# Kernel tuning notes

Measured on AMD Instinct MI355X. Metric: run time of the kernel, lower is better.

Reference implementation:

```python
import jax, jax.numpy as jnp
import numpy as np

L, B, N, C, H = 8, 8, 512, 1024, 16
D = C // H
TP = (2.0 * D) ** 0.5  # temperature_coeff * head_dim, sqrt


def _ln(x):
    # LayerNorm(eps=1e-6, no affine)
    m = jnp.mean(x, axis=-1, keepdims=True)
    v = jnp.var(x, axis=-1, keepdims=True)
    return (x - m) * jax.lax.rsqrt(v + 1e-6)


def _modulate(x, shift, scale):
    return x * (1 + scale) + shift


def setup_inputs() -> dict:
    key = jax.random.key(0)
    ks = jax.random.split(key, 18)
    s = 0.02
    return {
        "x": jax.random.normal(ks[0], (B, N, C), dtype=jnp.float32),
        "time": jax.random.uniform(ks[1], (B, 1), dtype=jnp.float32) * 100.0,
        "label": jax.random.normal(ks[2], (B, 2), dtype=jnp.float32),
        "x_mask": jax.random.randint(ks[3], (B, N, 1), 0, 2).astype(jnp.float32),
        # ValueLabelEmbed: Linear(2 -> C)
        "Wl": jax.random.normal(ks[4], (C, 2), dtype=jnp.float32) * s,
        "bl": jnp.zeros((C,), dtype=jnp.float32),
        # per-layer stacked weights (leading dim L)
        "Wq": jax.random.normal(ks[5], (L, C, C), dtype=jnp.float32) * s,
        "Wk": jax.random.normal(ks[6], (L, C, C), dtype=jnp.float32) * s,
        "Wv": jax.random.normal(ks[7], (L, C, C), dtype=jnp.float32) * s,
        "W1": jax.random.normal(ks[8], (L, 4 * C, C), dtype=jnp.float32) * s,
        "b1": jnp.zeros((L, 4 * C), dtype=jnp.float32),
        "W2": jax.random.normal(ks[9], (L, C, 4 * C), dtype=jnp.float32) * s,
        "b2": jnp.zeros((L, C), dtype=jnp.float32),
        "Wm": jax.random.normal(ks[10], (L, 6 * C, C), dtype=jnp.float32) * s,
        "bm": jnp.zeros((L, 6 * C), dtype=jnp.float32),
        # FinalLayer
        "Wf": jax.random.normal(ks[11], (C, C), dtype=jnp.float32) * s,
        "bf": jnp.zeros((C,), dtype=jnp.float32),
        "Wmf": jax.random.normal(ks[12], (2 * C, C), dtype=jnp.float32) * s,
        "bmf": jnp.zeros((2 * C,), dtype=jnp.float32),
    }


def reference(x, time, label, x_mask, Wl, bl, Wq, Wk, Wv, W1, b1, W2, b2, Wm, bm, Wf, bf, Wmf, bmf):
    # ValueLabelEmbed: (B,2) -> (B,1,C)
    lemb = (label @ Wl.T + bl)[:, None, :]
    # TimeEmbedding: interleaved sin/cos of time / 10000^(2i/d)
    base = jnp.power(10000.0, 2.0 * jnp.arange(C, dtype=jnp.float32) / C)
    te = time / base  # (B, C)
    even = (jnp.arange(C) % 2) == 0
    te = jnp.where(even, jnp.sin(te), jnp.cos(te))
    c = lemb + te[:, None, :]  # (B,1,C)

    # self-attention mask: True where exactly one of the pair is valid
    xm = x_mask[:, :, 0]  # (B,N)
    mask = ((xm[:, :, None] + xm[:, None, :]) == 1.0)[:, None, :, :]  # (B,1,N,N)

    def block(xc, p):
        wq, wk, wv, w1, bb1, w2, bb2, wm, bbm = p
        m6 = jax.nn.selu(c) @ wm.T + bbm  # (B,1,6C)
        sm, sc, gm, sf, cf, gf = jnp.split(m6, 6, axis=-1)
        h = _modulate(_ln(xc), sm, sc) * x_mask
        q = (h @ wq.T).reshape(B, N, H, D)
        k = (h @ wk.T).reshape(B, N, H, D)
        v = (h @ wv.T).reshape(B, N, H, D)
        scores = jnp.einsum('bqhd,bkhd->bhqk', q, k) / TP
        scores = jnp.where(mask, -jnp.inf, scores)
        alpha = jax.nn.softmax(scores, axis=-1)
        att = jnp.einsum('bhqk,bkhd->bqhd', alpha, v).reshape(B, N, C)
        xc = xc + gm * att
        h2 = _modulate(_ln(xc), sf, cf)
        ffn = jax.nn.selu(h2 @ w1.T + bb1) @ w2.T + bb2
        xc = (xc + gf * ffn) * x_mask
        return xc, None

    x, _ = jax.lax.scan(block, x, (Wq, Wk, Wv, W1, b1, W2, b2, Wm, bm))

    # FinalLayer
    m2 = jax.nn.selu(c) @ Wmf.T + bmf
    shift, scale = jnp.split(m2, 2, axis=-1)
    out = (_modulate(_ln(x), shift, scale) @ Wf.T + bf) * x_mask
    return out
```

## Files before the change

### kernel.cpp

```cpp
#include <hip/hip_runtime.h>
#include <hip/hip_bf16.h>
#include <cstddef>

#define DEVI __device__ __forceinline__

typedef __attribute__((ext_vector_type(4))) float f4v;
typedef __attribute__((ext_vector_type(16))) float f16v;
typedef __attribute__((ext_vector_type(8))) short s8v;
typedef __attribute__((ext_vector_type(4))) short s4v;

using bf16 = __hip_bfloat16;

constexpr float SELU_A = 1.6732632423543772f;
constexpr float SELU_S = 1.0507009873554805f;
constexpr float TPINV  = 0.08838834764831845f;

DEVI float bfbits(short s) { return __uint_as_float(((unsigned)(unsigned short)s) << 16); }
DEVI unsigned short f2bu(float f) {
  bf16 h = __float2bfloat16(f);
  return __builtin_bit_cast(unsigned short, h);
}
DEVI float seluf(float x) { return x > 0.f ? SELU_S * x : SELU_S * SELU_A * (__expf(x) - 1.f); }

DEVI void gl16(const void* g, void* l) {
  __builtin_amdgcn_global_load_lds((__attribute__((address_space(1))) void*)g,
                                   (__attribute__((address_space(3))) void*)l, 16, 0, 0);
}

DEVI void conv8(const float* __restrict__ src, bf16* __restrict__ dst) {
  f4v a = *(const f4v*)src;
  f4v b = *(const f4v*)(src + 4);
  s8v o;
  #pragma unroll
  for (int j = 0; j < 4; j++) { o[j] = (short)f2bu(a[j]); o[4 + j] = (short)f2bu(b[j]); }
  *(s8v*)dst = o;
}

__global__ void k_compact(const float* __restrict__ xm, int* __restrict__ idx,
                          int* __restrict__ pos, int* __restrict__ cnt,
                          int* __restrict__ start, int* __restrict__ t2b)
{
  int t = threadIdx.x;
  int b = t >> 6, lane = t & 63;
  __shared__ int scnt[8];
  int base = b * 512 + lane * 8;
  int mb[8]; int lc = 0;
  #pragma unroll
  for (int i = 0; i < 8; i++) { mb[i] = (xm[base + i] != 0.f) ? 1 : 0; lc += mb[i]; }
  int s = lc;
  #pragma unroll
  for (int o = 1; o < 64; o <<= 1) { int tt = __shfl_up(s, o); if (lane >= o) s += tt; }
  int run = s - lc;
  #pragma unroll
  for (int i = 0; i < 8; i++) {
    int n = lane * 8 + i;
    if (mb[i]) { idx[b * 512 + run] = n; pos[b * 512 + n] = run; run++; }
    else pos[b * 512 + n] = -1;
  }
  if (lane == 63) scnt[b] = s;
  __syncthreads();
  if (t == 0) {
    int st = 0, tile = 0;
    for (int bb = 0; bb < 8; bb++) {
      cnt[bb] = scnt[bb];
      start[bb] = st;
      int nt = (scnt[bb] + 127) >> 7;
      for (int k = 0; k < nt * 2; k++) t2b[tile++] = bb;
      st += nt * 128;
    }
    start[8] = st;
    for (; tile < 64; tile++) t2b[tile] = 0;
  }
}

__global__ __launch_bounds__(256) void k_prolog(
    const float* __restrict__ xin, const int* __restrict__ idx, const int* __restrict__ cnt,
    const int* __restrict__ start, const int* __restrict__ t2b, float* __restrict__ xc,
    const float* __restrict__ wq, const float* __restrict__ wk, const float* __restrict__ wv,
    const float* __restrict__ w1, const float* __restrict__ w2,
    bf16* __restrict__ wqkvb, bf16* __restrict__ w1b, bf16* __restrict__ w2b,
    const float* __restrict__ cs, const float* __restrict__ Wm, const float* __restrict__ bm,
    float* __restrict__ mAll, const float* __restrict__ Wmf, const float* __restrict__ bmf,
    float* __restrict__ m2v)
{
  int bid = blockIdx.x, t = threadIdx.x;
  __shared__ float cls[8192];
  if (bid < 4096) {
    int row = bid;
    if (row >= start[8]) return;
    int tb = t2b[row >> 6], slot = row - start[tb];
    f4v v = {0.f, 0.f, 0.f, 0.f};
    if (slot < cnt[tb])
      v = *(const f4v*)&xin[((size_t)tb * 512 + idx[tb * 512 + slot]) * 1024 + t * 4];
    *(f4v*)&xc[(size_t)row * 1024 + t * 4] = v;
  } else if (bid < 9728) {
    int i = (bid - 4096) * 256 + t;
    if (i < 393216) {
      int o = i * 8;
      int row = o >> 10, col = o & 1023;
      int sel = row >> 10, sr = row & 1023;
      conv8((sel == 0 ? wq : sel == 1 ? wk : wv) + (size_t)sr * 1024 + col, wqkvb + o);
    } else if (i < 917504) {
      size_t o = (size_t)(i - 393216) * 8;
      conv8(w1 + o, w1b + o);
    } else {
      size_t o = (size_t)(i - 917504) * 8;
      conv8(w2 + o, w2b + o);
    }
  } else {
    int mode = (bid < 22016) ? 0 : 1;
    const float* W = mode ? Wmf : Wm;
    const float* bias = mode ? bmf : bm;
    float* out = mode ? m2v : mAll;
    int O = mode ? 2048 : 49152;
    int ob = mode ? (bid - 22016) : (bid - 9728);
    #pragma unroll
    for (int i = 0; i < 8; i++)
      *(f4v*)&cls[i * 1024 + t * 4] = *(const f4v*)&cs[i * 1024 + t * 4];
    __syncthreads();
    int w = t >> 6, l = t & 63;
    int o = ob * 4 + w;
    if (o >= O) return;
    const float* Wr = W + (size_t)o * 1024;
    f4v wv[4];
    #pragma unroll
    for (int i = 0; i < 4; i++) wv[i] = *(const f4v*)&Wr[i * 256 + l * 4];
    float acc[8] = {0.f, 0.f, 0.f, 0.f, 0.f, 0.f, 0.f, 0.f};
    #pragma unroll
    for (int i = 0; i < 4; i++) {
      #pragma unroll
      for (int b = 0; b < 8; b++) {
        f4v cv = *(const f4v*)&cls[b * 1024 + i * 256 + l * 4];
        acc[b] += wv[i][0] * cv[0] + wv[i][1] * cv[1] + wv[i][2] * cv[2] + wv[i][3] * cv[3];
      }
    }
    #pragma unroll
    for (int b = 0; b < 8; b++) {
      #pragma unroll
      for (int off = 32; off; off >>= 1) acc[b] += __shfl_xor(acc[b], off);
    }
    float bv = bias[o];
    #pragma unroll
    for (int b = 0; b < 8; b++) {
      if (l == b) {
        float val = acc[b] + bv;
        size_t dst;
        if (mode == 0) { int ll = o / 6144, ft = o - ll * 6144; dst = ((size_t)ll * 8 + b) * 6144 + ft; }
        else dst = (size_t)b * 2048 + o;
        out[dst] = val;
      }
    }
  }
}

__global__ __launch_bounds__(256) void k_scatter(const float* __restrict__ ffin,
    const int* __restrict__ pos, const int* __restrict__ start, float* __restrict__ out)
{
  int row = blockIdx.x, t = threadIdx.x, b = row >> 9;
  int p = pos[row];
  f4v v = {0.f, 0.f, 0.f, 0.f};
  if (p >= 0) v = *(const f4v*)&ffin[(size_t)(start[b] + p) * 1024 + t * 4];
  *(f4v*)&out[(size_t)row * 1024 + t * 4] = v;
}

__global__ void k_cond(const float* __restrict__ tim, const float* __restrict__ lab,
                       const float* __restrict__ Wl, const float* __restrict__ bl,
                       float* __restrict__ cs)
{
  int b = blockIdx.x, t = threadIdx.x;
  float l0 = lab[b * 2 + 0], l1 = lab[b * 2 + 1], tv = tim[b];
  #pragma unroll
  for (int i = 0; i < 4; i++) {
    int j = t + 256 * i;
    float e = powf(10000.f, (2.f * (float)j) * (1.f / 1024.f));
    float arg = tv / e;
    float te = ((j & 1) == 0) ? sinf(arg) : cosf(arg);
    float c = l0 * Wl[j * 2 + 0] + l1 * Wl[j * 2 + 1] + bl[j] + te;
    cs[b * 1024 + j] = seluf(c);
  }
}

__global__ __launch_bounds__(256) void k_lnmod(
    const float* __restrict__ x, const float* __restrict__ shiftB, const float* __restrict__ scaleB,
    int bstride, const int* __restrict__ cnt, const int* __restrict__ start,
    const int* __restrict__ t2b, bf16* __restrict__ out)
{
  int row = blockIdx.x, t = threadIdx.x;
  if (row >= start[8]) return;
  int tb = t2b[row >> 6], slot = row - start[tb];
  if (slot >= cnt[tb]) {
    s4v z = {0, 0, 0, 0};
    *(s4v*)&out[(size_t)row * 1024 + t * 4] = z;
    return;
  }
  const float* xr = x + (size_t)row * 1024;
  f4v v = *(const f4v*)&xr[t * 4];
  float s = v[0] + v[1] + v[2] + v[3];
  float ss = v[0]*v[0] + v[1]*v[1] + v[2]*v[2] + v[3]*v[3];
  #pragma unroll
  for (int off = 32; off; off >>= 1) { s += __shfl_xor(s, off); ss += __shfl_xor(ss, off); }
  __shared__ float rs[4], rss[4];
  int w = t >> 6;
  if ((t & 63) == 0) { rs[w] = s; rss[w] = ss; }
  __syncthreads();
  s = rs[0] + rs[1] + rs[2] + rs[3];
  ss = rss[0] + rss[1] + rss[2] + rss[3];
  float mean = s * (1.f / 1024.f);
  float var = ss * (1.f / 1024.f) - mean * mean;
  float rstd = rsqrtf(var + 1e-6f);
  f4v sh = *(const f4v*)&shiftB[(size_t)tb * bstride + t * 4];
  f4v sc = *(const f4v*)&scaleB[(size_t)tb * bstride + t * 4];
  s4v o;
  #pragma unroll
  for (int i = 0; i < 4; i++)
    o[i] = (short)f2bu((v[i] - mean) * rstd * (1.f + sc[i]) + sh[i]);
  *(s4v*)&out[(size_t)row * 1024 + t * 4] = o;
}

__global__ __launch_bounds__(256) void k_resid(
    float* __restrict__ x, const bf16* __restrict__ att, const float* __restrict__ m6b,
    const int* __restrict__ cnt, const int* __restrict__ start,
    const int* __restrict__ t2b, bf16* __restrict__ h2)
{
  int row = blockIdx.x, t = threadIdx.x;
  if (row >= start[8]) return;
  int tb = t2b[row >> 6], slot = row - start[tb];
  if (slot >= cnt[tb]) {
    s4v z = {0, 0, 0, 0};
    *(s4v*)&h2[(size_t)row * 1024 + t * 4] = z;
    return;
  }
  float* xr = x + (size_t)row * 1024;
  const float* gm = m6b + (size_t)tb * 6144 + 2048;
  const float* sf = m6b + (size_t)tb * 6144 + 3072;
  const float* cf = m6b + (size_t)tb * 6144 + 4096;
  f4v xv = *(const f4v*)&xr[t * 4];
  s4v av = *(const s4v*)&att[((size_t)tb * 512 + slot) * 1024 + t * 4];
  f4v gv = *(const f4v*)&gm[t * 4];
  f4v vv;
  #pragma unroll
  for (int i = 0; i < 4; i++) vv[i] = xv[i] + gv[i] * bfbits(av[i]);
  *(f4v*)&xr[t * 4] = vv;
  float s = vv[0] + vv[1] + vv[2] + vv[3];
  float ss = vv[0]*vv[0] + vv[1]*vv[1] + vv[2]*vv[2] + vv[3]*vv[3];
  #pragma unroll
  for (int off = 32; off; off >>= 1) { s += __shfl_xor(s, off); ss += __shfl_xor(ss, off); }
  __shared__ float rs[4], rss[4];
  int w = t >> 6;
  if ((t & 63) == 0) { rs[w] = s; rss[w] = ss; }
  __syncthreads();
  s = rs[0] + rs[1] + rs[2] + rs[3];
  ss = rss[0] + rss[1] + rss[2] + rss[3];
  float mean = s * (1.f / 1024.f);
  float var = ss * (1.f / 1024.f) - mean * mean;
  float rstd = rsqrtf(var + 1e-6f);
  f4v sfv = *(const f4v*)&sf[t * 4];
  f4v cfv = *(const f4v*)&cf[t * 4];
  s4v o;
  #pragma unroll
  for (int i = 0; i < 4; i++)
    o[i] = (short)f2bu((vv[i] - mean) * rstd * (1.f + cfv[i]) + sfv[i]);
  *(s4v*)&h2[(size_t)row * 1024 + t * 4] = o;
}

__global__ __launch_bounds__(256) void k_attn(
    const bf16* __restrict__ q, const bf16* __restrict__ k, const bf16* __restrict__ vt,
    const int* __restrict__ cnt, bf16* __restrict__ att,
    const float* __restrict__ nwq, const float* __restrict__ nwk, const float* __restrict__ nwv,
    const float* __restrict__ nw1, const float* __restrict__ nw2,
    bf16* __restrict__ dqkv, bf16* __restrict__ dw1, bf16* __restrict__ dw2, int mode)
{
  if (blockIdx.x >= 4) {
    int cid = (blockIdx.x - 4) * 128 + blockIdx.y;
    int i0 = cid * 256 + threadIdx.x;
    #pragma unroll
    for (int half = 0; half < 2; half++) {
      int j = i0 * 2 + half;
      if (mode == 1) {
        if (j < 131072) conv8(nwq + (size_t)j * 8, dqkv + (size_t)j * 8);
      } else {
        if (j < 393216) {
          int o = j * 8;
          int row = o >> 10, col = o & 1023;
          int sel = row >> 10, sr = row & 1023;
          conv8((sel == 0 ? nwq : sel == 1 ? nwk : nwv) + (size_t)sr * 1024 + col, dqkv + o);
        } else if (j < 917504) {
          size_t o = (size_t)(j - 393216) * 8;
          conv8(nw1 + o, dw1 + o);
        } else {
          size_t o = (size_t)(j - 917504) * 8;
          conv8(nw2 + o, dw2 + o);
        }
      }
    }
    return;
  }

  int bh = blockIdx.y, b = bh >> 4, hh = bh & 15;
  int cntb = cnt[b];
  if ((int)blockIdx.x * 128 >= cntb) return;
  int t = threadIdx.x, w = t >> 6, lane = t & 63;
  int fr = lane & 15, g = lane >> 4;
  int qw = blockIdx.x * 128 + w * 32;
  const size_t ho = (size_t)bh * (512 * 64);

  __shared__ bf16 Pb[4][32][72];

  s8v qf[2][2];
  #pragma unroll
  for (int mf = 0; mf < 2; mf++)
    #pragma unroll
    for (int kk = 0; kk < 2; kk++)
      qf[mf][kk] = *(const s8v*)(q + ho + (size_t)(qw + mf * 16 + fr) * 64 + kk * 32 + g * 8);

  float mrow[2][4], lsum[2][4];
  f4v oacc[2][4];
  const f4v vzero = {0.f, 0.f, 0.f, 0.f};
  #pragma unroll
  for (int mf = 0; mf < 2; mf++)
    #pragma unroll
    for (int r = 0; r < 4; r++) { mrow[mf][r] = -3.0e38f; lsum[mf][r] = 0.f; }
  #pragma unroll
  for (int mf = 0; mf < 2; mf++)
    #pragma unroll
    for (int nd = 0; nd < 4; nd++) oacc[mf][nd] = vzero;

  int nkt = (cntb + 63) >> 6;
  for (int kt = 0; kt < nkt; kt++) {
    int kb0 = kt * 64;
    f4v sacc[2][4];
    #pragma unroll
    for (int mf = 0; mf < 2; mf++)
      #pragma unroll
      for (int nf = 0; nf < 4; nf++) sacc[mf][nf] = vzero;
    #pragma unroll
    for (int kk = 0; kk < 2; kk++) {
      s8v kf[4];
      #pragma unroll
      for (int nf = 0; nf < 4; nf++)
        kf[nf] = *(const s8v*)(k + ho + (size_t)(kb0 + nf * 16 + fr) * 64 + kk * 32 + g * 8);
      #pragma unroll
      for (int mf = 0; mf < 2; mf++)
        #pragma unroll
        for (int nf = 0; nf < 4; nf++)
          sacc[mf][nf] = __builtin_amdgcn_mfma_f32_16x16x32_bf16(qf[mf][kk], kf[nf], sacc[mf][nf], 0, 0, 0);
    }
    #pragma unroll
    for (int mf = 0; mf < 2; mf++) {
      #pragma unroll
      for (int r = 0; r < 4; r++) {
        float mx = -3.0e38f;
        #pragma unroll
        for (int nf = 0; nf < 4; nf++) {
          float s = sacc[mf][nf][r] * TPINV;
          if (kb0 + nf * 16 + fr >= cntb) s = -1.0e30f;
          sacc[mf][nf][r] = s;
          mx = fmaxf(mx, s);
        }
        mx = fmaxf(mx, __shfl_xor(mx, 1));
        mx = fmaxf(mx, __shfl_xor(mx, 2));
        mx = fmaxf(mx, __shfl_xor(mx, 4));
        mx = fmaxf(mx, __shfl_xor(mx, 8));
        float mnew = fmaxf(mrow[mf][r], mx);
        float corr = __expf(mrow[mf][r] - mnew);
        mrow[mf][r] = mnew;
        float ps = 0.f;
        #pragma unroll
        for (int nf = 0; nf < 4; nf++) {
          float p = __expf(sacc[mf][nf][r] - mnew);
          ps += p;
          Pb[w][mf * 16 + g * 4 + r][nf * 16 + fr] = __float2bfloat16(p);
        }
        lsum[mf][r] = lsum[mf][r] * corr + ps;
        #pragma unroll
        for (int nd = 0; nd < 4; nd++) oacc[mf][nd][r] *= corr;
      }
    }
    #pragma unroll
    for (int kk = 0; kk < 2; kk++) {
      s8v pf[2], vf[4];
      #pragma unroll
      for (int mf = 0; mf < 2; mf++)
        pf[mf] = *(const s8v*)&Pb[w][mf * 16 + fr][kk * 32 + g * 8];
      #pragma unroll
      for (int nd = 0; nd < 4; nd++)
        vf[nd] = *(const s8v*)(vt + ho + (size_t)(nd * 16 + fr) * 512 + kb0 + kk * 32 + g * 8);
      #pragma unroll
      for (int mf = 0; mf < 2; mf++)
        #pragma unroll
        for (int nd = 0; nd < 4; nd++)
          oacc[mf][nd] = __builtin_amdgcn_mfma_f32_16x16x32_bf16(pf[mf], vf[nd], oacc[mf][nd], 0, 0, 0);
    }
  }
  float inv[2][4];
  #pragma unroll
  for (int mf = 0; mf < 2; mf++)
    #pragma unroll
    for (int r = 0; r < 4; r++) {
      float ls = lsum[mf][r];
      ls += __shfl_xor(ls, 1);
      ls += __shfl_xor(ls, 2);
      ls += __shfl_xor(ls, 4);
      ls += __shfl_xor(ls, 8);
      inv[mf][r] = 1.f / ls;
    }
  #pragma unroll
  for (int mf = 0; mf < 2; mf++)
    #pragma unroll
    for (int nd = 0; nd < 4; nd++)
      #pragma unroll
      for (int r = 0; r < 4; r++) {
        int row = qw + mf * 16 + g * 4 + r;
        att[(size_t)(b * 512 + row) * 1024 + hh * 64 + nd * 16 + fr] =
            __float2bfloat16(oacc[mf][nd][r] * inv[mf][r]);
      }
}

template <int EPI, int BM, int BN>
__global__ __launch_bounds__(256) void k_gemm(
    const bf16* __restrict__ A, const bf16* __restrict__ W,
    const float* __restrict__ bias, int Kst, int kLen, int Ncols,
    const int* __restrict__ cnt, const int* __restrict__ start, const int* __restrict__ t2b,
    bf16* __restrict__ outb, float* __restrict__ outf)
{
  constexpr int MFR = BM / 64;
  constexpr int NFR = BN / 64;
  constexpr int NA  = BM / 32;
  constexpr int NW  = BN / 32;
  __shared__ bf16 As[BM][64];
  __shared__ bf16 Ws[BN][64];
  int t = threadIdx.x, lane = t & 63, w = t >> 6;
  int wr = w >> 1, wc = w & 1;
  int m0 = blockIdx.y * BM, n0 = blockIdx.x * BN;
  if (m0 >= start[8]) return;
  int kOff = blockIdx.z * kLen;
  int r32 = lane & 31, hi = lane >> 5;

  const bf16* Abase = A + (size_t)m0 * Kst + kOff;
  const bf16* Wbase = W + (size_t)n0 * Kst + kOff;

  f16v acc[MFR][NFR];
  #pragma unroll
  for (int i = 0; i < MFR; i++)
    #pragma unroll
    for (int j = 0; j < NFR; j++)
      #pragma unroll
      for (int e = 0; e < 16; e++) acc[i][j][e] = 0.f;

  int nkt = kLen >> 6;
  for (int kt = 0; kt < nkt; kt++) {
    int k0 = kt << 6;
    __syncthreads();
    #pragma unroll
    for (int i = 0; i < NA; i++) {
      int Z = w * (NA * 1024) + i * 1024 + lane * 16;
      int row = Z >> 7, slot = (Z >> 4) & 7;
      int ss = slot ^ (row & 7);
      gl16(Abase + (size_t)row * Kst + k0 + ss * 8, (char*)As + Z);
    }
    #pragma unroll
    for (int i = 0; i < NW; i++) {
      int Z = w * (NW * 1024) + i * 1024 + lane * 16;
      int row = Z >> 7, slot = (Z >> 4) & 7;
      int ss = slot ^ (row & 7);
      gl16(Wbase + (size_t)row * Kst + k0 + ss * 8, (char*)Ws + Z);
    }
    __syncthreads();
    #pragma unroll
    for (int kk = 0; kk < 4; kk++) {
      s8v af[MFR], bfr[NFR];
      #pragma unroll
      for (int mf = 0; mf < MFR; mf++) {
        int row = wr * (BM / 2) + mf * 32 + r32;
        int sl = (kk * 2 + hi) ^ (row & 7);
        af[mf] = *(const s8v*)((const char*)As + row * 128 + sl * 16);
      }
      #pragma unroll
      for (int nf = 0; nf < NFR; nf++) {
        int row = wc * (BN / 2) + nf * 32 + r32;
        int sl = (kk * 2 + hi) ^ (row & 7);
        bfr[nf] = *(const s8v*)((const char*)Ws + row * 128 + sl * 16);
      }
      #pragma unroll
      for (int mf = 0; mf < MFR; mf++)
        #pragma unroll
        for (int nf = 0; nf < NFR; nf++)
          acc[mf][nf] = __builtin_amdgcn_mfma_f32_32x32x16_bf16(af[mf], bfr[nf], acc[mf][nf], 0, 0, 0);
    }
  }

  int tb = t2b[m0 >> 6];
  int sb = start[tb];
  #pragma unroll
  for (int mf = 0; mf < MFR; mf++) {
    #pragma unroll
    for (int nf = 0; nf < NFR; nf++) {
      int col = n0 + wc * (BN / 2) + nf * 32 + r32;
      #pragma unroll
      for (int qd = 0; qd < 4; qd++) {
        int row0 = m0 + wr * (BM / 2) + mf * 32 + qd * 8 + hi * 4;
        if (EPI == 0) {
          int sel = col >> 10, cl = col & 1023;
          int nn = row0 - sb;
          int h2 = cl >> 6, dd = cl & 63;
          if (sel == 2) {
            s4v o4;
            #pragma unroll
            for (int r = 0; r < 4; r++) o4[r] = (short)f2bu(acc[mf][nf][qd * 4 + r]);
            *(s4v*)&outb[(size_t)2 * 4194304 + (((size_t)tb * 16 + h2) * 64 + dd) * 512 + nn] = o4;
          } else {
            #pragma unroll
            for (int r = 0; r < 4; r++)
              outb[(size_t)sel * 4194304 + (((size_t)tb * 16 + h2) * 512 + (nn + r)) * 64 + dd] =
                  __float2bfloat16(acc[mf][nf][qd * 4 + r]);
          }
        } else {
          #pragma unroll
          for (int r = 0; r < 4; r++) {
            int row = row0 + r;
            float val = acc[mf][nf][qd * 4 + r];
            if (EPI == 1) {
              outb[(size_t)row * Ncols + col] = __float2bfloat16(seluf(val + bias[col]));
            } else if (EPI == 3) {
              outf[(size_t)row * 1024 + col] = val + bias[col];
            } else {
              outb[(size_t)blockIdx.z * 4194304 + (size_t)row * 1024 + col] = __float2bfloat16(val);
            }
          }
        }
      }
    }
  }
}

__global__ __launch_bounds__(256) void k_comb(
    const bf16* __restrict__ part, const float* __restrict__ bias,
    const float* __restrict__ gfb, const float* __restrict__ shiftN,
    const float* __restrict__ scaleN, int strideN,
    float* __restrict__ x, const int* __restrict__ cnt, const int* __restrict__ start,
    const int* __restrict__ t2b, bf16* __restrict__ h)
{
  int row = blockIdx.x, t = threadIdx.x;
  if (row >= start[8]) return;
  int tb = t2b[row >> 6], slot = row - start[tb];
  if (slot >= cnt[tb]) return;
  size_t o = (size_t)row * 1024 + t * 4;
  f4v sum = {0.f, 0.f, 0.f, 0.f};
  #pragma unroll
  for (int p = 0; p < 8; p++) {
    s4v pv = *(const s4v*)&part[o + (size_t)p * 4194304];
    #pragma unroll
    for (int i = 0; i < 4; i++) sum[i] += bfbits(pv[i]);
  }
  f4v bv = *(const f4v*)&bias[t * 4];
  f4v gf = *(const f4v*)&gfb[(size_t)tb * 6144 + t * 4];
  f4v xv = *(const f4v*)&x[o];
  f4v vv;
  #pragma unroll
  for (int i = 0; i < 4; i++)
    vv[i] = xv[i] + gf[i] * (sum[i] + bv[i]);
  *(f4v*)&x[o] = vv;
  float s = vv[0] + vv[1] + vv[2] + vv[3];
  float ss = vv[0]*vv[0] + vv[1]*vv[1] + vv[2]*vv[2] + vv[3]*vv[3];
  #pragma unroll
  for (int off = 32; off; off >>= 1) { s += __shfl_xor(s, off); ss += __shfl_xor(ss, off); }
  __shared__ float rs[4], rss[4];
  int w = t >> 6;
  if ((t & 63) == 0) { rs[w] = s; rss[w] = ss; }
  __syncthreads();
  s = rs[0] + rs[1] + rs[2] + rs[3];
  ss = rss[0] + rss[1] + rss[2] + rss[3];
  float mean = s * (1.f / 1024.f);
  float var = ss * (1.f / 1024.f) - mean * mean;
  float rstd = rsqrtf(var + 1e-6f);
  f4v sh = *(const f4v*)&shiftN[(size_t)tb * strideN + t * 4];
  f4v sc = *(const f4v*)&scaleN[(size_t)tb * strideN + t * 4];
  s4v ho;
  #pragma unroll
  for (int i = 0; i < 4; i++)
    ho[i] = (short)f2bu((vv[i] - mean) * rstd * (1.f + sc[i]) + sh[i]);
  *(s4v*)&h[(size_t)row * 1024 + t * 4] = ho;
}

extern "C" void kernel_launch(void* const* d_in, const int* in_sizes, int n_in,
                              void* d_out, int out_size, void* d_ws, size_t ws_size,
                              hipStream_t stream)
{
  const float* x_in  = (const float*)d_in[0];
  const float* tim   = (const float*)d_in[1];
  const float* lab   = (const float*)d_in[2];
  const float* xmask = (const float*)d_in[3];
  const float* Wl  = (const float*)d_in[4];
  const float* bl  = (const float*)d_in[5];
  const float* Wq  = (const float*)d_in[6];
  const float* Wk  = (const float*)d_in[7];
  const float* Wv  = (const float*)d_in[8];
  const float* W1  = (const float*)d_in[9];
  const float* b1  = (const float*)d_in[10];
  const float* W2  = (const float*)d_in[11];
  const float* b2  = (const float*)d_in[12];
  const float* Wm  = (const float*)d_in[13];
  const float* bm  = (const float*)d_in[14];
  const float* Wf  = (const float*)d_in[15];
  const float* bfp = (const float*)d_in[16];
  const float* Wmf = (const float*)d_in[17];
  const float* bmf = (const float*)d_in[18];

  char* ws = (char*)d_ws;
  float* x     = (float*)(ws + 0);
  float* cs    = (float*)(ws + 16777216);
  float* mAll  = (float*)(ws + 16809984);
  float* m2v   = (float*)(ws + 18382848);
  bf16*  h     = (bf16*)(ws + 18448384);
  bf16*  qb    = (bf16*)(ws + 26836992);
  bf16*  kb    = (bf16*)(ws + 35225600);
  bf16*  vb    = (bf16*)(ws + 43614208);
  bf16*  att   = (bf16*)(ws + 52002816);
  bf16*  f1    = (bf16*)(ws + 60391424);
  bf16*  wqkv0 = (bf16*)(ws + 93945856);
  bf16*  w1b0  = (bf16*)(ws + 100237312);
  bf16*  w2b0  = (bf16*)(ws + 108625920);
  bf16*  wfb   = (bf16*)(ws + 117014528);
  float* ffin  = (float*)(ws + 119111680);
  int*   idxb  = (int*)(ws + 135888896);
  int*   posb  = (int*)(ws + 135905280);
  int*   cntb  = (int*)(ws + 135921664);
  int*   strtb = (int*)(ws + 135921728);
  int*   t2bb  = (int*)(ws + 135921792);
  bf16*  wqkv1 = (bf16*)(ws + 135925760);
  bf16*  w1b1  = (bf16*)(ws + 142217216);
  bf16*  w2b1  = (bf16*)(ws + 150605824);
  bf16*  part  = (bf16*)(ws + 158994432);

  bf16* wqkvS[2] = { wqkv0, wqkv1 };
  bf16* w1S[2]   = { w1b0, w1b1 };
  bf16* w2S[2]   = { w2b0, w2b1 };

  k_compact<<<1, 512, 0, stream>>>(xmask, idxb, posb, cntb, strtb, t2bb);
  k_cond<<<8, 256, 0, stream>>>(tim, lab, Wl, bl, cs);
  k_prolog<<<22528, 256, 0, stream>>>(x_in, idxb, cntb, strtb, t2bb, x,
                                      Wq, Wk, Wv, W1, W2, wqkv0, w1b0, w2b0,
                                      cs, Wm, bm, mAll, Wmf, bmf, m2v);
  k_lnmod<<<4096, 256, 0, stream>>>(x, mAll + 0, mAll + 1024, 6144, cntb, strtb, t2bb, h);

  for (int l = 0; l < 8; l++) {
    const float* m6b = mAll + (size_t)l * 49152;
    int sel = l & 1, nsel = sel ^ 1;
    int last = (l == 7);

    k_gemm<0, 128, 64><<<dim3(48, 32), 256, 0, stream>>>(h, wqkvS[sel], nullptr, 1024, 1024, 3072,
                                                         cntb, strtb, t2bb, qb, nullptr);
    if (!last) {
      k_attn<<<dim3(26, 128), 256, 0, stream>>>(qb, kb, vb, cntb, att,
          Wq + (size_t)(l + 1) * 1048576, Wk + (size_t)(l + 1) * 1048576,
          Wv + (size_t)(l + 1) * 1048576, W1 + (size_t)(l + 1) * 4194304,
          W2 + (size_t)(l + 1) * 4194304,
          wqkvS[nsel], w1S[nsel], w2S[nsel], 0);
    } else {
      k_attn<<<dim3(26, 128), 256, 0, stream>>>(qb, kb, vb, cntb, att,
          Wf, Wf, Wf, Wf, Wf, wfb, wfb, wfb, 1);
    }
    k_resid<<<4096, 256, 0, stream>>>(x, att, m6b, cntb, strtb, t2bb, h);
    k_gemm<1, 128, 64><<<dim3(64, 32), 256, 0, stream>>>(h, w1S[sel], b1 + l * 4096, 1024, 1024, 4096,
                                                         cntb, strtb, t2bb, f1, nullptr);
    k_gemm<4, 128, 128><<<dim3(8, 32, 8), 256, 0, stream>>>(f1, w2S[sel], nullptr, 4096, 512, 1024,
                                                            cntb, strtb, t2bb, part, nullptr);
    const float* nShift = last ? m2v : (mAll + (size_t)(l + 1) * 49152);
    const float* nScale = last ? (m2v + 1024) : (mAll + (size_t)(l + 1) * 49152 + 1024);
    int nStride = last ? 2048 : 6144;
    k_comb<<<4096, 256, 0, stream>>>(part, b2 + l * 1024, m6b + 5120,
                                     nShift, nScale, nStride,
                                     x, cntb, strtb, t2bb, h);
  }

  k_gemm<3, 128, 64><<<dim3(16, 32), 256, 0, stream>>>(h, wfb, bfp, 1024, 1024, 1024,
                                                       cntb, strtb, t2bb, nullptr, ffin);
  k_scatter<<<4096, 256, 0, stream>>>(ffin, posb, strtb, (float*)d_out);
}
```

Measured before the change: 1.357 ms.

## Defer per-layer modulation matvecs into attention kernel and batch rows per wave

The prologue no longer computes all eight layers' modulation vectors (Wm @ selu(c)). It now computes only layer 0 and the final-layer vector. Each later layer's modulation matvec is computed by extra blocks appended to the previous layer's attention launch, alongside the bf16 weight conversions already placed there. The matvec helper also processes four output rows per wave instead of one, which cuts the number of blocks and how often the conditioning vector is staged into LDS. The shared-memory buffer is unified so the attention scratch and the conditioning vector share one allocation. The cost is more register pressure in the matvec and slightly larger attention grids.

```diff
diff --git a/kernel.cpp b/kernel.cpp
--- a/kernel.cpp
+++ b/kernel.cpp
@@ -34,6 +34,42 @@
   #pragma unroll
   for (int j = 0; j < 4; j++) { o[j] = (short)f2bu(a[j]); o[4 + j] = (short)f2bu(b[j]); }
   *(s8v*)dst = o;
+}
+
+DEVI void matvec16(const float* __restrict__ W, const float* __restrict__ bias,
+                   float* __restrict__ out, const float* cls, int base, int O, int stride)
+{
+  int t = threadIdx.x, w = t >> 6, l = t & 63;
+  int o0 = base + w * 4;
+  if (o0 >= O) return;
+  f4v wv[4][4];
+  #pragma unroll
+  for (int r = 0; r < 4; r++)
+    #pragma unroll
+    for (int i = 0; i < 4; i++)
+      wv[r][i] = *(const f4v*)&W[(size_t)(o0 + r) * 1024 + i * 256 + l * 4];
+  #pragma unroll
+  for (int r = 0; r < 4; r++) {
+    float acc[8] = {0.f, 0.f, 0.f, 0.f, 0.f, 0.f, 0.f, 0.f};
+    #pragma unroll
+    for (int i = 0; i < 4; i++) {
+      #pragma unroll
+      for (int b = 0; b < 8; b++) {
+        f4v cv = *(const f4v*)&cls[b * 1024 + i * 256 + l * 4];
+        acc[b] += wv[r][i][0] * cv[0] + wv[r][i][1] * cv[1] +
+                  wv[r][i][2] * cv[2] + wv[r][i][3] * cv[3];
+      }
+    }
+    #pragma unroll
+    for (int b = 0; b < 8; b++) {
+      #pragma unroll
+      for (int off = 32; off; off >>= 1) acc[b] += __shfl_xor(acc[b], off);
+    }
+    float bv = bias[o0 + r];
+    #pragma unroll
+    for (int b = 0; b < 8; b++)
+      if (l == b) out[(size_t)b * stride + o0 + r] = acc[b] + bv;
+  }
 }
 
 __global__ void k_compact(const float* __restrict__ xm, int* __restrict__ idx,
@@ -108,48 +144,14 @@
       conv8(w2 + o, w2b + o);
     }
   } else {
-    int mode = (bid < 22016) ? 0 : 1;
-    const float* W = mode ? Wmf : Wm;
-    const float* bias = mode ? bmf : bm;
-    float* out = mode ? m2v : mAll;
-    int O = mode ? 2048 : 49152;
-    int ob = mode ? (bid - 22016) : (bid - 9728);
     #pragma unroll
     for (int i = 0; i < 8; i++)
       *(f4v*)&cls[i * 1024 + t * 4] = *(const f4v*)&cs[i * 1024 + t * 4];
     __syncthreads();
-    int w = t >> 6, l = t & 63;
-    int o = ob * 4 + w;
-    if (o >= O) return;
-    const float* Wr = W + (size_t)o * 1024;
-    f4v wv[4];
-    #pragma unroll
-    for (int i = 0; i < 4; i++) wv[i] = *(const f4v*)&Wr[i * 256 + l * 4];
-    float acc[8] = {0.f, 0.f, 0.f, 0.f, 0.f, 0.f, 0.f, 0.f};
-    #pragma unroll
-    for (int i = 0; i < 4; i++) {
-      #pragma unroll
-      for (int b = 0; b < 8; b++) {
-        f4v cv = *(const f4v*)&cls[b * 1024 + i * 256 + l * 4];
-        acc[b] += wv[i][0] * cv[0] + wv[i][1] * cv[1] + wv[i][2] * cv[2] + wv[i][3] * cv[3];
-      }
-    }
-    #pragma unroll
-    for (int b = 0; b < 8; b++) {
-      #pragma unroll
-      for (int off = 32; off; off >>= 1) acc[b] += __shfl_xor(acc[b], off);
-    }
-    float bv = bias[o];
-    #pragma unroll
-    for (int b = 0; b < 8; b++) {
-      if (l == b) {
-        float val = acc[b] + bv;
-        size_t dst;
-        if (mode == 0) { int ll = o / 6144, ft = o - ll * 6144; dst = ((size_t)ll * 8 + b) * 6144 + ft; }
-        else dst = (size_t)b * 2048 + o;
-        out[dst] = val;
-      }
-    }
+    if (bid < 10112)
+      matvec16(Wm, bm, mAll, cls, (bid - 9728) * 16, 6144, 6144);
+    else
+      matvec16(Wmf, bmf, m2v, cls, (bid - 10112) * 16, 2048, 2048);
   }
 }
 
@@ -268,8 +270,23 @@
     const int* __restrict__ cnt, bf16* __restrict__ att,
     const float* __restrict__ nwq, const float* __restrict__ nwk, const float* __restrict__ nwv,
     const float* __restrict__ nw1, const float* __restrict__ nw2,
-    bf16* __restrict__ dqkv, bf16* __restrict__ dw1, bf16* __restrict__ dw2, int mode)
-{
+    bf16* __restrict__ dqkv, bf16* __restrict__ dw1, bf16* __restrict__ dw2, int mode,
+    const float* __restrict__ cs, const float* __restrict__ WmN,
+    const float* __restrict__ bmN, float* __restrict__ m6out)
+{
+  __shared__ __attribute__((aligned(16))) char smem[32768];
+  if (blockIdx.x >= 26) {
+    if (mode == 1) return;
+    float* cls = (float*)smem;
+    int t = threadIdx.x;
+    #pragma unroll
+    for (int i = 0; i < 8; i++)
+      *(f4v*)&cls[i * 1024 + t * 4] = *(const f4v*)&cs[i * 1024 + t * 4];
+    __syncthreads();
+    int mid = (blockIdx.x - 26) * 128 + blockIdx.y;
+    matvec16(WmN, bmN, m6out, cls, mid * 16, 6144, 6144);
+    return;
+  }
   if (blockIdx.x >= 4) {
     int cid = (blockIdx.x - 4) * 128 + blockIdx.y;
     int i0 = cid * 256 + threadIdx.x;
@@ -304,7 +321,8 @@
   int qw = blockIdx.x * 128 + w * 32;
   const size_t ho = (size_t)bh * (512 * 64);
 
-  __shared__ bf16 Pb[4][32][72];
+  typedef bf16 PbRow[32][72];
+  PbRow* Pb = (PbRow*)smem;
 
   s8v qf[2][2];
   #pragma unroll
@@ -638,7 +656,7 @@
 
   k_compact<<<1, 512, 0, stream>>>(xmask, idxb, posb, cntb, strtb, t2bb);
   k_cond<<<8, 256, 0, stream>>>(tim, lab, Wl, bl, cs);
-  k_prolog<<<22528, 256, 0, stream>>>(x_in, idxb, cntb, strtb, t2bb, x,
+  k_prolog<<<10240, 256, 0, stream>>>(x_in, idxb, cntb, strtb, t2bb, x,
                                       Wq, Wk, Wv, W1, W2, wqkv0, w1b0, w2b0,
                                       cs, Wm, bm, mAll, Wmf, bmf, m2v);
   k_lnmod<<<4096, 256, 0, stream>>>(x, mAll + 0, mAll + 1024, 6144, cntb, strtb, t2bb, h);
@@ -651,14 +669,17 @@
     k_gemm<0, 128, 64><<<dim3(48, 32), 256, 0, stream>>>(h, wqkvS[sel], nullptr, 1024, 1024, 3072,
                                                          cntb, strtb, t2bb, qb, nullptr);
     if (!last) {
-      k_attn<<<dim3(26, 128), 256, 0, stream>>>(qb, kb, vb, cntb, att,
+      k_attn<<<dim3(29, 128), 256, 0, stream>>>(qb, kb, vb, cntb, att,
           Wq + (size_t)(l + 1) * 1048576, Wk + (size_t)(l + 1) * 1048576,
           Wv + (size_t)(l + 1) * 1048576, W1 + (size_t)(l + 1) * 4194304,
           W2 + (size_t)(l + 1) * 4194304,
-          wqkvS[nsel], w1S[nsel], w2S[nsel], 0);
+          wqkvS[nsel], w1S[nsel], w2S[nsel], 0,
+          cs, Wm + (size_t)(l + 1) * 6291456, bm + (l + 1) * 6144,
+          mAll + (size_t)(l + 1) * 49152);
     } else {
-      k_attn<<<dim3(26, 128), 256, 0, stream>>>(qb, kb, vb, cntb, att,
-          Wf, Wf, Wf, Wf, Wf, wfb, wfb, wfb, 1);
+      k_attn<<<dim3(29, 128), 256, 0, stream>>>(qb, kb, vb, cntb, att,
+          Wf, Wf, Wf, Wf, Wf, wfb, wfb, wfb, 1,
+          cs, nullptr, nullptr, nullptr);
     }
     k_resid<<<4096, 256, 0, stream>>>(x, att, m6b, cntb, strtb, t2bb, h);
     k_gemm<1, 128, 64><<<dim3(64, 32), 256, 0, stream>>>(h, w1S[sel], b1 + l * 4096, 1024, 1024, 4096,
```

Measured after the change: 1.319 ms. 1.03x faster.
